# Optimization experiments

Measured on AMD Instinct MI355X. Metric: run time of the kernel, lower is better.

Reference implementation:

```python
import jax, jax.numpy as jnp
import numpy as np

N_NODES = 50000
N_EDGES = 800000
N_GRAPHS = 512
D = 128
NUM_LAYERS = 3
BN_EPS = 1e-5


def setup_inputs() -> dict:
    key = jax.random.key(0)
    ks = jax.random.split(key, 16)
    x = jax.random.normal(ks[0], (N_NODES, D), dtype=jnp.float32)
    edge_index = jax.random.randint(ks[1], (2, N_EDGES), 0, N_NODES, dtype=jnp.int64)
    batch = jnp.sort(jax.random.randint(ks[2], (N_NODES,), 0, N_GRAPHS, dtype=jnp.int64))
    # per-layer MLP params (all dims are 128 so we can stack across layers)
    s1 = 1.0 / np.sqrt(D)
    W1 = jax.random.uniform(ks[3], (NUM_LAYERS, D, D), jnp.float32, -s1, s1)
    b1 = jax.random.uniform(ks[4], (NUM_LAYERS, D), jnp.float32, -s1, s1)
    W2 = jax.random.uniform(ks[5], (NUM_LAYERS, D, D), jnp.float32, -s1, s1)
    b2 = jax.random.uniform(ks[6], (NUM_LAYERS, D), jnp.float32, -s1, s1)
    eps = jnp.zeros((NUM_LAYERS,), jnp.float32)  # train_eps=True, init 0.0
    gamma = jnp.ones((NUM_LAYERS, D), jnp.float32)
    beta = jnp.zeros((NUM_LAYERS, D), jnp.float32)
    return {"x": x, "edge_index": edge_index, "batch": batch,
            "W1": W1, "b1": b1, "W2": W2, "b2": b2,
            "eps": eps, "gamma": gamma, "beta": beta}


def _gin_forward(x, edge_index, batch, W1, b1, W2, b2, eps, gamma, beta):
    src, dst = edge_index[0], edge_index[1]
    h = x
    for i in range(NUM_LAYERS):
        # GINConv: MLP((1+eps)*h_i + sum_{j->i} h_j)  (scatter-add over edges)
        agg = jax.ops.segment_sum(h[src], dst, num_segments=N_NODES)
        z = (1.0 + eps[i]) * h + agg
        z = jax.nn.relu(z @ W1[i] + b1[i]) @ W2[i] + b2[i]
        # BatchNorm1d (training-mode batch stats, biased variance)
        mean = jnp.mean(z, axis=0)
        var = jnp.mean(jnp.square(z - mean), axis=0)
        h = (z - mean) * jax.lax.rsqrt(var + BN_EPS) * gamma[i] + beta[i]
        if i < NUM_LAYERS - 1:
            h = jax.nn.relu(h)  # dropout is identity in eval mode
    # global_mean_pool over batch segment ids
    sums = jax.ops.segment_sum(h, batch, num_segments=N_GRAPHS)
    counts = jax.ops.segment_sum(jnp.ones((N_NODES, 1), h.dtype), batch, num_segments=N_GRAPHS)
    return sums / jnp.maximum(counts, 1.0)


def reference(x, edge_index, batch, W1, b1, W2, b2, eps, gamma, beta):
    return _gin_forward(x, edge_index, batch, W1, b1, W2, b2, eps, gamma, beta)
```

## Files before the change

### kernel.cpp

```cpp
#include <hip/hip_runtime.h>

#define N_NODESC 50000
#define N_EDGESC 800000
#define N_GRAPHSC 512
#define DF 128
#define BN_EPSF 1e-5f
#define CSR_CAP 64
#define CUR_STRIDE 32
#define LAYER_BLOCKS 3125
#define NSLICE 32
#define POISON 0xAAAAAAAAu

#define PREP_SCAT_B 3125
#define PREP_CONVX_B 3125
#define PREP_CONVW_B 48
#define PREP_ZERO_B 6
#define PREP_TOTAL_B (PREP_SCAT_B + PREP_CONVX_B + PREP_CONVW_B + PREP_ZERO_B)

typedef _Float16 half8 __attribute__((ext_vector_type(8)));
typedef _Float16 half2v __attribute__((ext_vector_type(2)));
typedef float floatx4 __attribute__((ext_vector_type(4)));

__global__ __launch_bounds__(256) void k_prep(
    const int* __restrict__ src, const int* __restrict__ dst,
    unsigned* __restrict__ cursor, unsigned short* __restrict__ csr,
    const float* __restrict__ x, _Float16* __restrict__ h,
    const float* __restrict__ W1, const float* __restrict__ W2, half8* __restrict__ wf,
    float* __restrict__ pb2)
{
    int b = blockIdx.x;
    int tid = threadIdx.x;
    if (b < PREP_SCAT_B) {
        int e = b * 256 + tid;
        int d = dst[e];
        int sv = src[e];
        unsigned pos = atomicAdd(&cursor[(size_t)d * CUR_STRIDE], 1u) - POISON;
        if (pos < CSR_CAP) csr[d * CSR_CAP + pos] = (unsigned short)sv;
    } else if (b < PREP_SCAT_B + PREP_CONVX_B) {
        int i8 = (b - PREP_SCAT_B) * 256 + tid;
        const floatx4* x4 = (const floatx4*)x;
        floatx4 v0 = __builtin_nontemporal_load(&x4[i8 * 2]);
        floatx4 v1 = __builtin_nontemporal_load(&x4[i8 * 2 + 1]);
        half8 o;
        o[0] = (_Float16)v0[0]; o[1] = (_Float16)v0[1]; o[2] = (_Float16)v0[2]; o[3] = (_Float16)v0[3];
        o[4] = (_Float16)v1[0]; o[5] = (_Float16)v1[1]; o[6] = (_Float16)v1[2]; o[7] = (_Float16)v1[3];
        ((half8*)h)[i8] = o;
    } else if (b < PREP_SCAT_B + PREP_CONVX_B + PREP_CONVW_B) {
        int t = (b - PREP_SCAT_B - PREP_CONVX_B) * 256 + tid;
        int m = t >> 11;
        int p = t & 2047;
        int ntile = p >> 8;
        int ks = (p >> 6) & 3;
        int l = p & 63;
        int n = ntile * 16 + (l & 15);
        int kb = ks * 32 + (l >> 4) * 8;
        const float* W = (m < 3) ? (W1 + (size_t)m * DF * DF) : (W2 + (size_t)(m - 3) * DF * DF);
        half8 o;
#pragma unroll
        for (int j = 0; j < 8; j++) o[j] = (_Float16)W[(size_t)(kb + j) * DF + n];
        wf[t] = o;
    } else {
        int b2 = b - (PREP_SCAT_B + PREP_CONVX_B + PREP_CONVW_B);
        floatx4* p4 = (floatx4*)pb2;
        int base = (b2 * 256 + tid) * 4;
#pragma unroll
        for (int j = 0; j < 4; j++) p4[base + j] = (floatx4)(0.f);
    }
}

#define KBN_BLOCKS 256
__global__ __launch_bounds__(256) void k_bn(
    const float* __restrict__ pb, const float* __restrict__ gma, const float* __restrict__ bta,
    _Float16* __restrict__ zh)
{
    __shared__ float red2[256];
    __shared__ float scs[256];
    int tid = threadIdx.x;
    float s = 0.f;
#pragma unroll
    for (int sl = 0; sl < NSLICE; sl++) s += pb[sl * 256 + tid];
    red2[tid] = s;
    __syncthreads();
    if (tid < 128) {
        const float invN = 1.f / (float)N_NODESC;
        float m = red2[tid] * invN;
        float var = red2[128 + tid] * invN - m * m;
        float sc = gma[tid] * rsqrtf(var + BN_EPSF);
        scs[tid] = sc;
        scs[128 + tid] = bta[tid] - m * sc;
    }
    __syncthreads();
    int i0 = blockIdx.x * 256 + tid;
    int cb = (i0 & 15) * 8;
    float sc[8], of[8];
#pragma unroll
    for (int j = 0; j < 8; j++) { sc[j] = scs[cb + j]; of[j] = scs[128 + cb + j]; }
    half8* z8 = (half8*)zh;
    const int nch = N_NODESC * 16;
    for (int i = i0; i < nch; i += KBN_BLOCKS * 256) {
        half8 v = z8[i];
        half8 o;
#pragma unroll
        for (int j = 0; j < 8; j++) {
            float f = fmaf((float)v[j], sc[j], of[j]);
            o[j] = (_Float16)fmaxf(f, 0.f);
        }
        z8[i] = o;
    }
}

#define TSTRIDE 136
__global__ __launch_bounds__(1024) void k_layer(
    const _Float16* __restrict__ Hin, const unsigned* __restrict__ cursor,
    const unsigned short* __restrict__ csr,
    const float* __restrict__ epsArr, int layer,
    const half8* __restrict__ W1f, const float* __restrict__ b1,
    const half8* __restrict__ W2f, const float* __restrict__ b2,
    _Float16* __restrict__ Z, float* __restrict__ pbOut)
{
    __shared__ _Float16 At[16 * TSTRIDE];
    __shared__ _Float16 Bt[16 * TSTRIDE];
    const int tid = threadIdx.x;
    const int w = tid >> 6, lane = tid & 63;

    {
        int n = blockIdx.x * 16 + w;
        int g = lane >> 4, c16 = lane & 15;
        const half8* Hr8 = (const half8*)Hin;
        int myidx = (int)csr[n * CSR_CAP + lane];
        int deg = (int)(cursor[(size_t)n * CUR_STRIDE] - POISON);
        if (deg > CSR_CAP) deg = CSR_CAP;

        float a[8];
#pragma unroll
        for (int i = 0; i < 8; i++) a[i] = 0.f;
        if (g == 0) {
            half8 u = Hr8[(size_t)n * 16 + c16];
            float e1 = 1.0f + epsArr[layer];
#pragma unroll
            for (int i = 0; i < 8; i++) a[i] = e1 * (float)u[i];
        }
        int T = (deg + 15) >> 4;
        int k = g;
        for (int t = 0; t < T; t++, k += 16) {
            int m0 = __shfl(myidx, k);
            int m1 = __shfl(myidx, k + 4);
            int m2 = __shfl(myidx, k + 8);
            int m3 = __shfl(myidx, k + 12);
            bool ok0 = k < deg, ok1 = (k + 4) < deg, ok2 = (k + 8) < deg, ok3 = (k + 12) < deg;
            half8 u0 = Hr8[(size_t)(ok0 ? m0 : n) * 16 + c16];
            half8 u1 = Hr8[(size_t)(ok1 ? m1 : n) * 16 + c16];
            half8 u2 = Hr8[(size_t)(ok2 ? m2 : n) * 16 + c16];
            half8 u3 = Hr8[(size_t)(ok3 ? m3 : n) * 16 + c16];
            float f0 = ok0 ? 1.f : 0.f, f1 = ok1 ? 1.f : 0.f;
            float f2 = ok2 ? 1.f : 0.f, f3 = ok3 ? 1.f : 0.f;
#pragma unroll
            for (int i = 0; i < 8; i++) {
                a[i] = fmaf((float)u0[i], f0, a[i]);
                a[i] = fmaf((float)u1[i], f1, a[i]);
                a[i] = fmaf((float)u2[i], f2, a[i]);
                a[i] = fmaf((float)u3[i], f3, a[i]);
            }
        }
#pragma unroll
        for (int i = 0; i < 8; i++) {
            a[i] += __shfl_xor(a[i], 16);
            a[i] += __shfl_xor(a[i], 32);
        }
        if (g == 0) {
            half8 o;
#pragma unroll
            for (int i = 0; i < 8; i++) o[i] = (_Float16)a[i];
            *(half8*)&At[w * TSTRIDE + c16 * 8] = o;
        }
    }
    __syncthreads();

    const int q = lane >> 4, c = lane & 15;
    if (w < 8) {
        half8 af[4];
#pragma unroll
        for (int ks = 0; ks < 4; ks++)
            af[ks] = *(const half8*)&At[c * TSTRIDE + ks * 32 + q * 8];
        floatx4 acc = (floatx4)(0.0f);
#pragma unroll
        for (int ks = 0; ks < 4; ks++) {
            half8 wfr = W1f[(w * 4 + ks) * 64 + lane];
            acc = __builtin_amdgcn_mfma_f32_16x16x32_f16(af[ks], wfr, acc, 0, 0, 0);
        }
        float b = b1[w * 16 + c];
#pragma unroll
        for (int r = 0; r < 4; r++) {
            float vv = fmaxf(acc[r] + b, 0.f);
            Bt[(q * 4 + r) * TSTRIDE + w * 16 + c] = (_Float16)vv;
        }
    }
    __syncthreads();

    if (w < 8) {
        half8 bf[4];
#pragma unroll
        for (int ks = 0; ks < 4; ks++)
            bf[ks] = *(const half8*)&Bt[c * TSTRIDE + ks * 32 + q * 8];
        floatx4 acc2 = (floatx4)(0.0f);
#pragma unroll
        for (int ks = 0; ks < 4; ks++) {
            half8 wfr = W2f[(w * 4 + ks) * 64 + lane];
            acc2 = __builtin_amdgcn_mfma_f32_16x16x32_f16(bf[ks], wfr, acc2, 0, 0, 0);
        }
        float b = b2[w * 16 + c];
        float ls = 0.f, lq = 0.f;
#pragma unroll
        for (int r = 0; r < 4; r++) {
            float vv = acc2[r] + b;
            ls += vv;
            lq += vv * vv;
            At[(q * 4 + r) * TSTRIDE + w * 16 + c] = (_Float16)vv;
        }
        ls += __shfl_xor(ls, 16);
        ls += __shfl_xor(ls, 32);
        lq += __shfl_xor(lq, 16);
        lq += __shfl_xor(lq, 32);
        if (q == 0) {
            float* pbb = pbOut + (size_t)(blockIdx.x & (NSLICE - 1)) * 256;
            atomicAdd(&pbb[w * 16 + c], ls);
            atomicAdd(&pbb[128 + w * 16 + c], lq);
        }
    }
    __syncthreads();

    half2v vz = *(const half2v*)&At[w * TSTRIDE + 2 * lane];
    ((half2v*)Z)[(size_t)(blockIdx.x * 16 + w) * 64 + lane] = vz;
}

static __device__ int lbound(const int* __restrict__ a, int n, int key) {
    int lo = 0, hi = n;
    while (lo < hi) {
        int mid = (lo + hi) >> 1;
        if (a[mid] < key) lo = mid + 1; else hi = mid;
    }
    return lo;
}

__global__ __launch_bounds__(128) void k_pool(const _Float16* __restrict__ Z, const int* __restrict__ batch,
                                              const float* __restrict__ pbL2, const float* __restrict__ gamma,
                                              const float* __restrict__ beta, float* __restrict__ out) {
    __shared__ int bnds[2];
    int g = blockIdx.x, c = threadIdx.x;
    if (threadIdx.x == 0) {
        bnds[0] = lbound(batch, N_NODESC, g);
        bnds[1] = lbound(batch, N_NODESC, g + 1);
    }
    float su = 0.f, sq = 0.f;
#pragma unroll 8
    for (int sl = 0; sl < NSLICE; sl++) {
        su += pbL2[sl * 256 + c];
        sq += pbL2[sl * 256 + 128 + c];
    }
    __syncthreads();
    const float invN = 1.f / (float)N_NODESC;
    float m = su * invN;
    float v = sq * invN - m * m;
    float sc = gamma[c] * rsqrtf(v + BN_EPSF);
    float of = beta[c] - m * sc;
    int lo = bnds[0], hi = bnds[1];
    float s = 0.f;
    int r = lo;
    for (; r + 4 <= hi; r += 4) {
        s += (float)Z[(size_t)r * DF + c] + (float)Z[(size_t)(r + 1) * DF + c]
           + (float)Z[(size_t)(r + 2) * DF + c] + (float)Z[(size_t)(r + 3) * DF + c];
    }
    for (; r < hi; r++) s += (float)Z[(size_t)r * DF + c];
    int cnt = hi - lo;
    out[g * DF + c] = (cnt > 0) ? (s / (float)cnt) * sc + of : 0.f;
}

extern "C" void kernel_launch(void* const* d_in, const int* in_sizes, int n_in,
                              void* d_out, int out_size, void* d_ws, size_t ws_size,
                              hipStream_t stream) {
    const float* x     = (const float*)d_in[0];
    const int*   ei    = (const int*)d_in[1];
    const int*   batch = (const int*)d_in[2];
    const float* W1    = (const float*)d_in[3];
    const float* b1    = (const float*)d_in[4];
    const float* W2    = (const float*)d_in[5];
    const float* b2    = (const float*)d_in[6];
    const float* eps   = (const float*)d_in[7];
    const float* gamma = (const float*)d_in[8];
    const float* beta  = (const float*)d_in[9];
    float* out = (float*)d_out;

    char* ws = (char*)d_ws;
    size_t o = 0;
    auto alloc = [&](size_t bytes) -> char* {
        char* p = ws + o;
        o += (bytes + 255) & ~(size_t)255;
        return p;
    };
    unsigned* cursor = (unsigned*)alloc((size_t)N_NODESC * CUR_STRIDE * sizeof(unsigned));
    unsigned short* csr = (unsigned short*)alloc((size_t)N_NODESC * CSR_CAP * sizeof(unsigned short));
    float* pb2     = (float*)alloc((size_t)3 * NSLICE * 256 * sizeof(float));
    half8* wf      = (half8*)alloc((size_t)6 * 2048 * sizeof(half8));
    _Float16* za   = (_Float16*)alloc((size_t)N_NODESC * DF * sizeof(_Float16));
    _Float16* zb   = (_Float16*)alloc((size_t)N_NODESC * DF * sizeof(_Float16));
    _Float16* hbuf = zb;
    (void)ws_size; (void)in_sizes; (void)n_in; (void)out_size;

    const int* srcA = ei;
    const int* dstA = ei + N_EDGESC;

    k_prep<<<PREP_TOTAL_B, 256, 0, stream>>>(srcA, dstA, cursor, csr, x, hbuf, W1, W2, wf, pb2);

    k_layer<<<LAYER_BLOCKS, 1024, 0, stream>>>(
        hbuf, cursor, csr, eps, 0,
        wf + 0 * 2048, b1 + 0 * DF, wf + 3 * 2048, b2 + 0 * DF, za, pb2 + 0 * 8192);
    k_bn<<<KBN_BLOCKS, 256, 0, stream>>>(pb2 + 0 * 8192, gamma + 0 * DF, beta + 0 * DF, za);
    k_layer<<<LAYER_BLOCKS, 1024, 0, stream>>>(
        za, cursor, csr, eps, 1,
        wf + 1 * 2048, b1 + 1 * DF, wf + 4 * 2048, b2 + 1 * DF, zb, pb2 + 1 * 8192);
    k_bn<<<KBN_BLOCKS, 256, 0, stream>>>(pb2 + 1 * 8192, gamma + 1 * DF, beta + 1 * DF, zb);
    k_layer<<<LAYER_BLOCKS, 1024, 0, stream>>>(
        zb, cursor, csr, eps, 2,
        wf + 2 * 2048, b1 + 2 * DF, wf + 5 * 2048, b2 + 2 * DF, za, pb2 + 2 * 8192);
    k_pool<<<N_GRAPHSC, DF, 0, stream>>>(za, batch, pb2 + 2 * 8192, gamma + 2 * DF, beta + 2 * DF, out);
}
```

Baseline: 275.6 us.

## Halve layer block to 512 threads with two nodes per wave in gather

Each wave in the layer kernel now aggregates neighbours for two nodes instead of one, so blocks use 8 waves instead of 16. This removes the 8 idle waves during the MFMA phases, which now run on every wave, and sets a launch-bounds occupancy hint. Each wave processes 8 neighbours per iteration per node, bounded by the larger of the two degrees, so padding work can rise when degrees differ. CSR stores in the prep kernel also become nontemporal stores.

```diff
diff --git a/kernel.cpp b/kernel.cpp
--- a/kernel.cpp
+++ b/kernel.cpp
@@ -35,7 +35,8 @@
         int d = dst[e];
         int sv = src[e];
         unsigned pos = atomicAdd(&cursor[(size_t)d * CUR_STRIDE], 1u) - POISON;
-        if (pos < CSR_CAP) csr[d * CSR_CAP + pos] = (unsigned short)sv;
+        if (pos < CSR_CAP)
+            __builtin_nontemporal_store((unsigned short)sv, &csr[d * CSR_CAP + pos]);
     } else if (b < PREP_SCAT_B + PREP_CONVX_B) {
         int i8 = (b - PREP_SCAT_B) * 256 + tid;
         const floatx4* x4 = (const floatx4*)x;
@@ -110,7 +111,7 @@
 }
 
 #define TSTRIDE 136
-__global__ __launch_bounds__(1024) void k_layer(
+__global__ __launch_bounds__(512, 8) void k_layer(
     const _Float16* __restrict__ Hin, const unsigned* __restrict__ cursor,
     const unsigned short* __restrict__ csr,
     const float* __restrict__ epsArr, int layer,
@@ -124,60 +125,72 @@
     const int w = tid >> 6, lane = tid & 63;
 
     {
-        int n = blockIdx.x * 16 + w;
+        int n0 = blockIdx.x * 16 + w * 2, n1 = n0 + 1;
         int g = lane >> 4, c16 = lane & 15;
         const half8* Hr8 = (const half8*)Hin;
-        int myidx = (int)csr[n * CSR_CAP + lane];
-        int deg = (int)(cursor[(size_t)n * CUR_STRIDE] - POISON);
-        if (deg > CSR_CAP) deg = CSR_CAP;
-
-        float a[8];
-#pragma unroll
-        for (int i = 0; i < 8; i++) a[i] = 0.f;
+        int idx0 = (int)csr[n0 * CSR_CAP + lane];
+        int idx1 = (int)csr[n1 * CSR_CAP + lane];
+        int d0 = (int)(cursor[(size_t)n0 * CUR_STRIDE] - POISON);
+        int d1 = (int)(cursor[(size_t)n1 * CUR_STRIDE] - POISON);
+        if (d0 > CSR_CAP) d0 = CSR_CAP;
+        if (d1 > CSR_CAP) d1 = CSR_CAP;
+
+        float a0[8], a1[8];
+#pragma unroll
+        for (int i = 0; i < 8; i++) { a0[i] = 0.f; a1[i] = 0.f; }
         if (g == 0) {
-            half8 u = Hr8[(size_t)n * 16 + c16];
+            half8 u0 = Hr8[(size_t)n0 * 16 + c16];
+            half8 u1 = Hr8[(size_t)n1 * 16 + c16];
             float e1 = 1.0f + epsArr[layer];
 #pragma unroll
-            for (int i = 0; i < 8; i++) a[i] = e1 * (float)u[i];
-        }
-        int T = (deg + 15) >> 4;
+            for (int i = 0; i < 8; i++) {
+                a0[i] = e1 * (float)u0[i];
+                a1[i] = e1 * (float)u1[i];
+            }
+        }
+        int dmax = d0 > d1 ? d0 : d1;
+        int T = (dmax + 7) >> 3;
         int k = g;
-        for (int t = 0; t < T; t++, k += 16) {
-            int m0 = __shfl(myidx, k);
-            int m1 = __shfl(myidx, k + 4);
-            int m2 = __shfl(myidx, k + 8);
-            int m3 = __shfl(myidx, k + 12);
-            bool ok0 = k < deg, ok1 = (k + 4) < deg, ok2 = (k + 8) < deg, ok3 = (k + 12) < deg;
-            half8 u0 = Hr8[(size_t)(ok0 ? m0 : n) * 16 + c16];
-            half8 u1 = Hr8[(size_t)(ok1 ? m1 : n) * 16 + c16];
-            half8 u2 = Hr8[(size_t)(ok2 ? m2 : n) * 16 + c16];
-            half8 u3 = Hr8[(size_t)(ok3 ? m3 : n) * 16 + c16];
-            float f0 = ok0 ? 1.f : 0.f, f1 = ok1 ? 1.f : 0.f;
-            float f2 = ok2 ? 1.f : 0.f, f3 = ok3 ? 1.f : 0.f;
+        for (int t = 0; t < T; t++, k += 8) {
+            int m00 = __shfl(idx0, k);
+            int m01 = __shfl(idx0, k + 4);
+            int m10 = __shfl(idx1, k);
+            int m11 = __shfl(idx1, k + 4);
+            bool o00 = k < d0, o01 = (k + 4) < d0;
+            bool o10 = k < d1, o11 = (k + 4) < d1;
+            half8 u00 = Hr8[(size_t)(o00 ? m00 : n0) * 16 + c16];
+            half8 u01 = Hr8[(size_t)(o01 ? m01 : n0) * 16 + c16];
+            half8 u10 = Hr8[(size_t)(o10 ? m10 : n1) * 16 + c16];
+            half8 u11 = Hr8[(size_t)(o11 ? m11 : n1) * 16 + c16];
+            float f00 = o00 ? 1.f : 0.f, f01 = o01 ? 1.f : 0.f;
+            float f10 = o10 ? 1.f : 0.f, f11 = o11 ? 1.f : 0.f;
 #pragma unroll
             for (int i = 0; i < 8; i++) {
-                a[i] = fmaf((float)u0[i], f0, a[i]);
-                a[i] = fmaf((float)u1[i], f1, a[i]);
-                a[i] = fmaf((float)u2[i], f2, a[i]);
-                a[i] = fmaf((float)u3[i], f3, a[i]);
+                a0[i] = fmaf((float)u00[i], f00, a0[i]);
+                a0[i] = fmaf((float)u01[i], f01, a0[i]);
+                a1[i] = fmaf((float)u10[i], f10, a1[i]);
+                a1[i] = fmaf((float)u11[i], f11, a1[i]);
             }
         }
 #pragma unroll
         for (int i = 0; i < 8; i++) {
-            a[i] += __shfl_xor(a[i], 16);
-            a[i] += __shfl_xor(a[i], 32);
+            a0[i] += __shfl_xor(a0[i], 16);
+            a0[i] += __shfl_xor(a0[i], 32);
+            a1[i] += __shfl_xor(a1[i], 16);
+            a1[i] += __shfl_xor(a1[i], 32);
         }
         if (g == 0) {
-            half8 o;
-#pragma unroll
-            for (int i = 0; i < 8; i++) o[i] = (_Float16)a[i];
-            *(half8*)&At[w * TSTRIDE + c16 * 8] = o;
+            half8 o0, o1;
+#pragma unroll
+            for (int i = 0; i < 8; i++) { o0[i] = (_Float16)a0[i]; o1[i] = (_Float16)a1[i]; }
+            *(half8*)&At[(w * 2) * TSTRIDE + c16 * 8] = o0;
+            *(half8*)&At[(w * 2 + 1) * TSTRIDE + c16 * 8] = o1;
         }
     }
     __syncthreads();
 
     const int q = lane >> 4, c = lane & 15;
-    if (w < 8) {
+    {
         half8 af[4];
 #pragma unroll
         for (int ks = 0; ks < 4; ks++)
@@ -197,7 +210,7 @@
     }
     __syncthreads();
 
-    if (w < 8) {
+    {
         half8 bf[4];
 #pragma unroll
         for (int ks = 0; ks < 4; ks++)
@@ -229,8 +242,12 @@
     }
     __syncthreads();
 
-    half2v vz = *(const half2v*)&At[w * TSTRIDE + 2 * lane];
-    ((half2v*)Z)[(size_t)(blockIdx.x * 16 + w) * 64 + lane] = vz;
+#pragma unroll
+    for (int r = 0; r < 2; r++) {
+        int row = w * 2 + r;
+        half2v vz = *(const half2v*)&At[row * TSTRIDE + 2 * lane];
+        ((half2v*)Z)[(size_t)(blockIdx.x * 16 + row) * 64 + lane] = vz;
+    }
 }
 
 static __device__ int lbound(const int* __restrict__ a, int n, int key) {
@@ -311,15 +328,15 @@
 
     k_prep<<<PREP_TOTAL_B, 256, 0, stream>>>(srcA, dstA, cursor, csr, x, hbuf, W1, W2, wf, pb2);
 
-    k_layer<<<LAYER_BLOCKS, 1024, 0, stream>>>(
+    k_layer<<<LAYER_BLOCKS, 512, 0, stream>>>(
         hbuf, cursor, csr, eps, 0,
         wf + 0 * 2048, b1 + 0 * DF, wf + 3 * 2048, b2 + 0 * DF, za, pb2 + 0 * 8192);
     k_bn<<<KBN_BLOCKS, 256, 0, stream>>>(pb2 + 0 * 8192, gamma + 0 * DF, beta + 0 * DF, za);
-    k_layer<<<LAYER_BLOCKS, 1024, 0, stream>>>(
+    k_layer<<<LAYER_BLOCKS, 512, 0, stream>>>(
         za, cursor, csr, eps, 1,
         wf + 1 * 2048, b1 + 1 * DF, wf + 4 * 2048, b2 + 1 * DF, zb, pb2 + 1 * 8192);
     k_bn<<<KBN_BLOCKS, 256, 0, stream>>>(pb2 + 1 * 8192, gamma + 1 * DF, beta + 1 * DF, zb);
-    k_layer<<<LAYER_BLOCKS, 1024, 0, stream>>>(
+    k_layer<<<LAYER_BLOCKS, 512, 0, stream>>>(
         zb, cursor, csr, eps, 2,
         wf + 2 * 2048, b1 + 2 * DF, wf + 5 * 2048, b2 + 2 * DF, za, pb2 + 2 * 8192);
     k_pool<<<N_GRAPHSC, DF, 0, stream>>>(za, batch, pb2 + 2 * 8192, gamma + 2 * DF, beta + 2 * DF, out);
```

Measured after the change: 269.7 us. 2.2% less time.
